# Performance work log

Hardware: AMD Instinct MI355X
Metric: run time of the kernel (lower is better)

Reference implementation:

```python
import jax, jax.numpy as jnp
import numpy as np

NUM_EXPERTS = 8
HIDDEN = 2048
EXPERT_DIM = 2048  # intermediate_size per shard (tp_size=1)
TOTAL_TOKENS = 32768  # divisible by NUM_EXPERTS


def setup_inputs() -> dict:
    key = jax.random.key(0)
    k1, k2, k3 = jax.random.split(key, 3)
    hidden_states = jax.random.normal(k1, (TOTAL_TOKENS, HIDDEN), dtype=jnp.float32)
    # (E, H, 2*D): gate and up projections concatenated on last dim
    gate_up_proj = jax.random.normal(k2, (NUM_EXPERTS, HIDDEN, 2 * EXPERT_DIM), dtype=jnp.float32) * 0.02
    # (E, D, H)
    down_proj = jax.random.normal(k3, (NUM_EXPERTS, EXPERT_DIM, HIDDEN), dtype=jnp.float32) * 0.02
    return {"hidden_states": hidden_states, "gate_up_proj": gate_up_proj, "down_proj": down_proj}


def reference(hidden_states, gate_up_proj, down_proj):
    E, H = gate_up_proj.shape[0], gate_up_proj.shape[1]
    # tokens are pre-sorted per expert: (E, T, H)
    x = hidden_states.reshape(E, -1, H)
    # grouped GEMM: (E,T,H) @ (E,H,2D) -> (E,T,2D)
    gate_up = jnp.einsum('eth,ehd->etd', x, gate_up_proj)
    gate, up = jnp.split(gate_up, 2, axis=-1)
    # SwiGLU epilogue then down projection: (E,T,D) @ (E,D,H) -> (E,T,H)
    act = up * jax.nn.silu(gate)
    out = jnp.einsum('etd,edh->eth', act, down_proj)
    # tp_size=1 -> all_reduce is identity
    return out.reshape(-1, H)
```

## Files before the change

kernel.cpp:

```cpp
#include <hip/hip_runtime.h>


#define E_EXPERTS 8
#define TPE 4096
#define KD 2048

typedef __bf16 bf16_t;
typedef __bf16 bf16x4 __attribute__((ext_vector_type(4)));
typedef __bf16 bf16x8 __attribute__((ext_vector_type(8)));
typedef float f32x4 __attribute__((ext_vector_type(4)));

#define GLOAD16(src, dst)                                               \
  __builtin_amdgcn_global_load_lds(                                     \
      (const __attribute__((address_space(1))) void*)(src),             \
      (__attribute__((address_space(3))) void*)(dst), 16, 0, 0)

__device__ inline void transpose64(const float* __restrict__ Wp,
                                   bf16_t* __restrict__ Tp, int N, int K,
                                   int n0, int k0, float (*tile)[65]) {
  const int rr = threadIdx.x >> 4;
  const int cc = (threadIdx.x & 15) * 4;
#pragma unroll
  for (int p = 0; p < 4; ++p) {
    const int k = rr + p * 16;
    float4 v = *(const float4*)(Wp + (size_t)(k0 + k) * N + n0 + cc);
    tile[k][cc + 0] = v.x;
    tile[k][cc + 1] = v.y;
    tile[k][cc + 2] = v.z;
    tile[k][cc + 3] = v.w;
  }
  __syncthreads();
#pragma unroll
  for (int p = 0; p < 4; ++p) {
    const int n = rr + p * 16;
    bf16x4 o;
#pragma unroll
    for (int q = 0; q < 4; ++q) o[q] = (bf16_t)tile[cc + q][n];
    *(bf16x4*)(Tp + (size_t)(n0 + n) * K + k0 + cc) = o;
  }
}

__global__ __launch_bounds__(256) void prep_kernel(
    const float* __restrict__ hs, bf16_t* __restrict__ xb,
    const float* __restrict__ w1, bf16_t* __restrict__ w1t,
    const float* __restrict__ w2, bf16_t* __restrict__ w2t) {
  __shared__ float tile[64][65];
  const int b = blockIdx.x;
  if (b < 16384) {
    const int nx = b & 63, ky = (b >> 6) & 31, e = b >> 11;
    transpose64(w1 + (size_t)e * KD * 4096, w1t + (size_t)e * 4096 * KD, 4096,
                KD, nx * 64, ky * 64, tile);
  } else if (b < 24576) {
    const int j = b - 16384;
    const int nx = j & 31, ky = (j >> 5) & 31, e = j >> 10;
    transpose64(w2 + (size_t)e * KD * KD, w2t + (size_t)e * KD * KD, KD, KD,
                nx * 64, ky * 64, tile);
  } else {
    const long n4 = (long)E_EXPERTS * TPE * KD / 4;
    long i = (long)(b - 24576) * blockDim.x + threadIdx.x;
    const long stride = 2048L * 256;
    const float4* in4 = (const float4*)hs;
    bf16x4* out4 = (bf16x4*)xb;
    for (; i < n4; i += stride) {
      float4 v = in4[i];
      bf16x4 o = {(bf16_t)v.x, (bf16_t)v.y, (bf16_t)v.z, (bf16_t)v.w};
      out4[i] = o;
    }
  }
}

template <bool FUSED, int NTN>
__global__ __launch_bounds__(512, 4) void moe_gemm_tlp_kernel(
    const bf16_t* __restrict__ A, const bf16_t* __restrict__ Bm,
    void* __restrict__ Cout) {
  constexpr int NT = KD / 32;

  __shared__ alignas(16) bf16_t As[3][64][64];
  __shared__ alignas(16) bf16_t Bs[3][128][64];

  const int NWG = gridDim.x;
  int wg = blockIdx.x;
  wg = (wg & 7) * (NWG >> 3) + (wg >> 3);
  const int e = wg / (32 * NTN);
  const int rem = wg % (32 * NTN);
  const int mt = rem / NTN, ntile = rem % NTN;
  const int t0 = mt * 128, n0 = ntile * 256;

  const int tid = threadIdx.x;
  const int wid = tid >> 6, lane = tid & 63;
  const int wr = wid >> 2, wc = wid & 3;

  const bf16_t* Ae = A + (size_t)e * TPE * KD + (size_t)t0 * KD;
  const bf16_t* Be = Bm + (size_t)e * (size_t)(FUSED ? 4096 : 2048) * KD;

  const int sp = lane >> 3;
  const int lc = lane & 7;

  const int pAr = wid * 8 + sp;
  const int cAr = lc ^ (pAr & 7);
  const bf16_t* aSrc = Ae + (size_t)(pAr + 64 * (cAr >> 2)) * KD + (cAr & 3) * 8;

  const bf16_t* bSrc[2];
#pragma unroll
  for (int i = 0; i < 2; ++i) {
    const int p = wid * 16 + i * 8 + sp;
    const int c = lc ^ (p & 7);
    const int R = n0 + p + 128 * (c >> 2);
    int srow;
    if constexpr (FUSED)
      srow = ((R >> 5) << 4) + (R & 15) + ((R >> 4) & 1) * 2048;
    else
      srow = R;
    bSrc[i] = Be + (size_t)srow * KD + (c & 3) * 8;
  }

  auto stageA = [&](int kt, int slot) {
    const int k0 = (kt & (NT - 1)) * 32;
    GLOAD16(aSrc + k0, &As[slot][wid * 8][0]);
  };
  auto stageB = [&](int kt, int slot) {
    const int k0 = (kt & (NT - 1)) * 32;
#pragma unroll
    for (int i = 0; i < 2; ++i)
      GLOAD16(bSrc[i] + k0, &Bs[slot][wid * 16 + i * 8][0]);
  };

  const int la = lane & 15, kg4 = lane >> 4;

  const bf16_t* pA[4];
#pragma unroll
  for (int m = 0; m < 4; ++m) {
    const int r = wr * 64 + m * 16 + la;
    const int p = r & 63, h = r >> 6;
    const int c = (h * 4 + kg4) ^ (p & 7);
    pA[m] = &As[0][p][c * 8];
  }
  const bf16_t* pB[4];
#pragma unroll
  for (int q = 0; q < 2; ++q)
#pragma unroll
    for (int jf = 0; jf < 2; ++jf) {
      const int R = wc * 64 + q * 32 + jf * 16 + la;
      const int p = R & 127, h = R >> 7;
      const int c = (h * 4 + kg4) ^ (p & 7);
      pB[q * 2 + jf] = &Bs[0][p][c * 8];
    }

  f32x4 acc[4][4] = {};
  bf16x8 am[4];
  bf16x8 bn[2];

#define W0 asm volatile("s_waitcnt lgkmcnt(0)" ::: "memory")
#define VMC3 asm volatile("s_waitcnt vmcnt(3)" ::: "memory")
#define BAR __builtin_amdgcn_s_barrier()
#define SCHED0 __builtin_amdgcn_sched_barrier(0)
#define PRIO1 __builtin_amdgcn_s_setprio(1)
#define PRIO0 __builtin_amdgcn_s_setprio(0)

#define TILE(t, S, S2)                                                       \
  do {                                                                       \
    am[0] = *(const bf16x8*)(pA[0] + (S) * 4096);                            \
    am[1] = *(const bf16x8*)(pA[1] + (S) * 4096);                            \
    am[2] = *(const bf16x8*)(pA[2] + (S) * 4096);                            \
    am[3] = *(const bf16x8*)(pA[3] + (S) * 4096);                            \
    bn[0] = *(const bf16x8*)(pB[0] + (S) * 8192);                            \
    bn[1] = *(const bf16x8*)(pB[1] + (S) * 8192);                            \
    stageA((t) + 2, S2);                                                     \
    stageB((t) + 2, S2);                                                     \
    W0; SCHED0;                                                              \
    PRIO1;                                                                   \
    _Pragma("unroll") for (int m = 0; m < 4; ++m) {                          \
      acc[m][0] = __builtin_amdgcn_mfma_f32_16x16x32_bf16(am[m], bn[0],      \
                                                          acc[m][0], 0, 0, 0); \
      acc[m][1] = __builtin_amdgcn_mfma_f32_16x16x32_bf16(am[m], bn[1],      \
                                                          acc[m][1], 0, 0, 0); \
    }                                                                        \
    PRIO0;                                                                   \
    bn[0] = *(const bf16x8*)(pB[2] + (S) * 8192);                            \
    bn[1] = *(const bf16x8*)(pB[3] + (S) * 8192);                            \
    W0; SCHED0;                                                              \
    PRIO1;                                                                   \
    _Pragma("unroll") for (int m = 0; m < 4; ++m) {                          \
      acc[m][2] = __builtin_amdgcn_mfma_f32_16x16x32_bf16(am[m], bn[0],      \
                                                          acc[m][2], 0, 0, 0); \
      acc[m][3] = __builtin_amdgcn_mfma_f32_16x16x32_bf16(am[m], bn[1],      \
                                                          acc[m][3], 0, 0, 0); \
    }                                                                        \
    PRIO0;                                                                   \
    VMC3;                                                                    \
    BAR; SCHED0;                                                             \
  } while (0)

  stageA(0, 0); stageB(0, 0);
  stageA(1, 1); stageB(1, 1);
  VMC3;
  BAR; SCHED0;

  int t = 0;
  for (; t < NT - 3; t += 3) {
    TILE(t, 0, 2);
    TILE(t + 1, 1, 0);
    TILE(t + 2, 2, 1);
  }
  TILE(t, 0, 2);

  const int rbase = t0 + wr * 64;
  if constexpr (FUSED) {
    bf16_t* Cp = (bf16_t*)Cout + (size_t)e * TPE * KD;
    const int jb = (n0 >> 1) + 32 * wc;
#pragma unroll
    for (int m = 0; m < 4; ++m)
#pragma unroll
      for (int q = 0; q < 2; ++q)
#pragma unroll
        for (int r = 0; r < 4; ++r) {
          const int row = rbase + m * 16 + kg4 * 4 + r;
          const int col = jb + q * 16 + la;
          const float g = acc[m][2 * q][r], u = acc[m][2 * q + 1][r];
          const float sg = 1.0f / (1.0f + __expf(-g));
          Cp[(size_t)row * KD + col] = (bf16_t)(u * g * sg);
        }
  } else {
    float* Cp = (float*)Cout + (size_t)e * TPE * KD;
#pragma unroll
    for (int m = 0; m < 4; ++m)
#pragma unroll
      for (int n = 0; n < 4; ++n)
#pragma unroll
        for (int r = 0; r < 4; ++r) {
          const int row = rbase + m * 16 + kg4 * 4 + r;
          const int col = n0 + wc * 64 + n * 16 + la;
          Cp[(size_t)row * KD + col] = acc[m][n][r];
        }
  }
#undef W0
#undef VMC3
#undef BAR
#undef SCHED0
#undef PRIO1
#undef PRIO0
#undef TILE
}

extern "C" void kernel_launch(void* const* d_in, const int* in_sizes, int n_in,
                              void* d_out, int out_size, void* d_ws,
                              size_t ws_size, hipStream_t stream) {
  const float* hs = (const float*)d_in[0];
  const float* w1 = (const float*)d_in[1];
  const float* w2 = (const float*)d_in[2];

  char* ws = (char*)d_ws;
  bf16_t* xb = (bf16_t*)(ws);
  bf16_t* w1t = (bf16_t*)(ws + (size_t)134217728);
  bf16_t* w2t = (bf16_t*)(ws + (size_t)268435456);
  bf16_t* act = (bf16_t*)(ws + (size_t)335544320);

  prep_kernel<<<26624, 256, 0, stream>>>(hs, xb, w1, w1t, w2, w2t);
  moe_gemm_tlp_kernel<true, 16><<<4096, 512, 0, stream>>>(xb, w1t, (void*)act);
  moe_gemm_tlp_kernel<false, 8><<<2048, 512, 0, stream>>>(act, w2t, d_out);
}
```

Before: 1.083 ms.

## Shrink GEMM tile to 128x128 with double-buffered LDS and higher occupancy

Reduces the per-workgroup output tile from 128x256 to 128x128 and switches from a triple-buffered to a double-buffered LDS pipeline with an extra barrier before staging. Launch bounds rise to 6 workgroups per CU and the grids double. The aim is more concurrent workgroups to hide latency. In exchange, each tile does less arithmetic per byte loaded, so global/LDS traffic per FLOP roughly rises, and the added barrier per k-step may cost throughput.

```diff
diff --git a/kernel.cpp b/kernel.cpp
--- a/kernel.cpp
+++ b/kernel.cpp
@@ -70,13 +70,13 @@
 }
 
 template <bool FUSED, int NTN>
-__global__ __launch_bounds__(512, 4) void moe_gemm_tlp_kernel(
+__global__ __launch_bounds__(512, 6) void moe_gemm128_kernel(
     const bf16_t* __restrict__ A, const bf16_t* __restrict__ Bm,
     void* __restrict__ Cout) {
   constexpr int NT = KD / 32;
 
-  __shared__ alignas(16) bf16_t As[3][64][64];
-  __shared__ alignas(16) bf16_t Bs[3][128][64];
+  __shared__ alignas(16) bf16_t As[2][64][64];
+  __shared__ alignas(16) bf16_t Bs[2][64][64];
 
   const int NWG = gridDim.x;
   int wg = blockIdx.x;
@@ -84,7 +84,7 @@
   const int e = wg / (32 * NTN);
   const int rem = wg % (32 * NTN);
   const int mt = rem / NTN, ntile = rem % NTN;
-  const int t0 = mt * 128, n0 = ntile * 256;
+  const int t0 = mt * 128, n0 = ntile * 128;
 
   const int tid = threadIdx.x;
   const int wid = tid >> 6, lane = tid & 63;
@@ -96,33 +96,25 @@
   const int sp = lane >> 3;
   const int lc = lane & 7;
 
-  const int pAr = wid * 8 + sp;
-  const int cAr = lc ^ (pAr & 7);
-  const bf16_t* aSrc = Ae + (size_t)(pAr + 64 * (cAr >> 2)) * KD + (cAr & 3) * 8;
-
-  const bf16_t* bSrc[2];
-#pragma unroll
-  for (int i = 0; i < 2; ++i) {
-    const int p = wid * 16 + i * 8 + sp;
-    const int c = lc ^ (p & 7);
-    const int R = n0 + p + 128 * (c >> 2);
+  const int pS = wid * 8 + sp;
+  const int cS = lc ^ (pS & 7);
+  const bf16_t* aSrc =
+      Ae + (size_t)(pS + 64 * (cS >> 2)) * KD + (cS & 3) * 8;
+  const bf16_t* bSrc;
+  {
+    const int R = n0 + pS + 64 * (cS >> 2);
     int srow;
     if constexpr (FUSED)
       srow = ((R >> 5) << 4) + (R & 15) + ((R >> 4) & 1) * 2048;
     else
       srow = R;
-    bSrc[i] = Be + (size_t)srow * KD + (c & 3) * 8;
-  }
-
-  auto stageA = [&](int kt, int slot) {
+    bSrc = Be + (size_t)srow * KD + (cS & 3) * 8;
+  }
+
+  auto stage = [&](int kt, int slot) {
     const int k0 = (kt & (NT - 1)) * 32;
     GLOAD16(aSrc + k0, &As[slot][wid * 8][0]);
-  };
-  auto stageB = [&](int kt, int slot) {
-    const int k0 = (kt & (NT - 1)) * 32;
-#pragma unroll
-    for (int i = 0; i < 2; ++i)
-      GLOAD16(bSrc[i] + k0, &Bs[slot][wid * 16 + i * 8][0]);
+    GLOAD16(bSrc + k0, &Bs[slot][wid * 8][0]);
   };
 
   const int la = lane & 15, kg4 = lane >> 4;
@@ -135,39 +127,37 @@
     const int c = (h * 4 + kg4) ^ (p & 7);
     pA[m] = &As[0][p][c * 8];
   }
-  const bf16_t* pB[4];
-#pragma unroll
-  for (int q = 0; q < 2; ++q)
-#pragma unroll
-    for (int jf = 0; jf < 2; ++jf) {
-      const int R = wc * 64 + q * 32 + jf * 16 + la;
-      const int p = R & 127, h = R >> 7;
-      const int c = (h * 4 + kg4) ^ (p & 7);
-      pB[q * 2 + jf] = &Bs[0][p][c * 8];
-    }
-
-  f32x4 acc[4][4] = {};
+  const bf16_t* pB[2];
+#pragma unroll
+  for (int nf = 0; nf < 2; ++nf) {
+    const int R = wc * 32 + nf * 16 + la;
+    const int p = R & 63, h = R >> 6;
+    const int c = (h * 4 + kg4) ^ (p & 7);
+    pB[nf] = &Bs[0][p][c * 8];
+  }
+
+  f32x4 acc[4][2] = {};
   bf16x8 am[4];
   bf16x8 bn[2];
 
 #define W0 asm volatile("s_waitcnt lgkmcnt(0)" ::: "memory")
-#define VMC3 asm volatile("s_waitcnt vmcnt(3)" ::: "memory")
+#define VMC2 asm volatile("s_waitcnt vmcnt(2)" ::: "memory")
 #define BAR __builtin_amdgcn_s_barrier()
 #define SCHED0 __builtin_amdgcn_sched_barrier(0)
 #define PRIO1 __builtin_amdgcn_s_setprio(1)
 #define PRIO0 __builtin_amdgcn_s_setprio(0)
 
-#define TILE(t, S, S2)                                                       \
+#define TILE(t, S)                                                           \
   do {                                                                       \
     am[0] = *(const bf16x8*)(pA[0] + (S) * 4096);                            \
     am[1] = *(const bf16x8*)(pA[1] + (S) * 4096);                            \
     am[2] = *(const bf16x8*)(pA[2] + (S) * 4096);                            \
     am[3] = *(const bf16x8*)(pA[3] + (S) * 4096);                            \
-    bn[0] = *(const bf16x8*)(pB[0] + (S) * 8192);                            \
-    bn[1] = *(const bf16x8*)(pB[1] + (S) * 8192);                            \
-    stageA((t) + 2, S2);                                                     \
-    stageB((t) + 2, S2);                                                     \
+    bn[0] = *(const bf16x8*)(pB[0] + (S) * 4096);                            \
+    bn[1] = *(const bf16x8*)(pB[1] + (S) * 4096);                            \
     W0; SCHED0;                                                              \
+    BAR;                                                                     \
+    stage((t) + 2, S);                                                       \
     PRIO1;                                                                   \
     _Pragma("unroll") for (int m = 0; m < 4; ++m) {                          \
       acc[m][0] = __builtin_amdgcn_mfma_f32_16x16x32_bf16(am[m], bn[0],      \
@@ -176,65 +166,49 @@
                                                           acc[m][1], 0, 0, 0); \
     }                                                                        \
     PRIO0;                                                                   \
-    bn[0] = *(const bf16x8*)(pB[2] + (S) * 8192);                            \
-    bn[1] = *(const bf16x8*)(pB[3] + (S) * 8192);                            \
-    W0; SCHED0;                                                              \
-    PRIO1;                                                                   \
-    _Pragma("unroll") for (int m = 0; m < 4; ++m) {                          \
-      acc[m][2] = __builtin_amdgcn_mfma_f32_16x16x32_bf16(am[m], bn[0],      \
-                                                          acc[m][2], 0, 0, 0); \
-      acc[m][3] = __builtin_amdgcn_mfma_f32_16x16x32_bf16(am[m], bn[1],      \
-                                                          acc[m][3], 0, 0, 0); \
-    }                                                                        \
-    PRIO0;                                                                   \
-    VMC3;                                                                    \
+    VMC2;                                                                    \
     BAR; SCHED0;                                                             \
   } while (0)
 
-  stageA(0, 0); stageB(0, 0);
-  stageA(1, 1); stageB(1, 1);
-  VMC3;
+  stage(0, 0);
+  stage(1, 1);
+  VMC2;
   BAR; SCHED0;
 
-  int t = 0;
-  for (; t < NT - 3; t += 3) {
-    TILE(t, 0, 2);
-    TILE(t + 1, 1, 0);
-    TILE(t + 2, 2, 1);
-  }
-  TILE(t, 0, 2);
+#pragma unroll 1
+  for (int t = 0; t < NT; t += 2) {
+    TILE(t, 0);
+    TILE(t + 1, 1);
+  }
 
   const int rbase = t0 + wr * 64;
   if constexpr (FUSED) {
     bf16_t* Cp = (bf16_t*)Cout + (size_t)e * TPE * KD;
-    const int jb = (n0 >> 1) + 32 * wc;
+    const int jb = ((n0 + wc * 32) >> 1) + la;
 #pragma unroll
     for (int m = 0; m < 4; ++m)
 #pragma unroll
-      for (int q = 0; q < 2; ++q)
+      for (int r = 0; r < 4; ++r) {
+        const int row = rbase + m * 16 + kg4 * 4 + r;
+        const float g = acc[m][0][r], u = acc[m][1][r];
+        const float sg = 1.0f / (1.0f + __expf(-g));
+        Cp[(size_t)row * KD + jb] = (bf16_t)(u * g * sg);
+      }
+  } else {
+    float* Cp = (float*)Cout + (size_t)e * TPE * KD;
+#pragma unroll
+    for (int m = 0; m < 4; ++m)
+#pragma unroll
+      for (int nf = 0; nf < 2; ++nf)
 #pragma unroll
         for (int r = 0; r < 4; ++r) {
           const int row = rbase + m * 16 + kg4 * 4 + r;
-          const int col = jb + q * 16 + la;
-          const float g = acc[m][2 * q][r], u = acc[m][2 * q + 1][r];
-          const float sg = 1.0f / (1.0f + __expf(-g));
-          Cp[(size_t)row * KD + col] = (bf16_t)(u * g * sg);
+          const int col = n0 + wc * 32 + nf * 16 + la;
+          Cp[(size_t)row * KD + col] = acc[m][nf][r];
         }
-  } else {
-    float* Cp = (float*)Cout + (size_t)e * TPE * KD;
-#pragma unroll
-    for (int m = 0; m < 4; ++m)
-#pragma unroll
-      for (int n = 0; n < 4; ++n)
-#pragma unroll
-        for (int r = 0; r < 4; ++r) {
-          const int row = rbase + m * 16 + kg4 * 4 + r;
-          const int col = n0 + wc * 64 + n * 16 + la;
-          Cp[(size_t)row * KD + col] = acc[m][n][r];
-        }
   }
 #undef W0
-#undef VMC3
+#undef VMC2
 #undef BAR
 #undef SCHED0
 #undef PRIO1
@@ -256,6 +230,6 @@
   bf16_t* act = (bf16_t*)(ws + (size_t)335544320);
 
   prep_kernel<<<26624, 256, 0, stream>>>(hs, xb, w1, w1t, w2, w2t);
-  moe_gemm_tlp_kernel<true, 16><<<4096, 512, 0, stream>>>(xb, w1t, (void*)act);
-  moe_gemm_tlp_kernel<false, 8><<<2048, 512, 0, stream>>>(act, w2t, d_out);
-}
+  moe_gemm128_kernel<true, 32><<<8192, 512, 0, stream>>>(xb, w1t, (void*)act);
+  moe_gemm128_kernel<false, 16><<<4096, 512, 0, stream>>>(act, w2t, d_out);
+}
```

After: 1.203 ms. 1.11x slower.

## Switch grouped GEMM inner loop to 32x32x16 bf16 MFMA tiles

Applied to the files above, without the earlier changes.

Replaces the 16x16x32 MFMA micro-tiles with 32x32x16 MFMA instructions, so each wave holds four 16-wide accumulators instead of sixteen 4-wide ones. The fused gate/up row interleave goes from 16-row to 32-row groups to match the new output fragment layout. LDS fragment loads are issued all at once with a partial lgkmcnt wait to overlap the second k-half. The goal is fewer LDS reads and MFMA issues per FLOP, with higher per-instruction latency and a different register and epilogue store pattern as the trade-off.

```diff
diff --git a/kernel.cpp b/kernel.cpp
--- a/kernel.cpp
+++ b/kernel.cpp
@@ -8,7 +8,7 @@
 typedef __bf16 bf16_t;
 typedef __bf16 bf16x4 __attribute__((ext_vector_type(4)));
 typedef __bf16 bf16x8 __attribute__((ext_vector_type(8)));
-typedef float f32x4 __attribute__((ext_vector_type(4)));
+typedef float f32x16 __attribute__((ext_vector_type(16)));
 
 #define GLOAD16(src, dst)                                               \
   __builtin_amdgcn_global_load_lds(                                     \
@@ -108,7 +108,7 @@
     const int R = n0 + p + 128 * (c >> 2);
     int srow;
     if constexpr (FUSED)
-      srow = ((R >> 5) << 4) + (R & 15) + ((R >> 4) & 1) * 2048;
+      srow = ((R >> 6) << 5) + (R & 31) + ((R >> 5) & 1) * 2048;
     else
       srow = R;
     bSrc[i] = Be + (size_t)srow * KD + (c & 3) * 8;
@@ -125,67 +125,69 @@
       GLOAD16(bSrc[i] + k0, &Bs[slot][wid * 16 + i * 8][0]);
   };
 
-  const int la = lane & 15, kg4 = lane >> 4;
-
-  const bf16_t* pA[4];
-#pragma unroll
-  for (int m = 0; m < 4; ++m) {
-    const int r = wr * 64 + m * 16 + la;
-    const int p = r & 63, h = r >> 6;
-    const int c = (h * 4 + kg4) ^ (p & 7);
-    pA[m] = &As[0][p][c * 8];
-  }
-  const bf16_t* pB[4];
-#pragma unroll
-  for (int q = 0; q < 2; ++q)
-#pragma unroll
-    for (int jf = 0; jf < 2; ++jf) {
-      const int R = wc * 64 + q * 32 + jf * 16 + la;
+  const int l31 = lane & 31, hk = lane >> 5;
+
+  const bf16_t* pA[2][2];
+#pragma unroll
+  for (int mf = 0; mf < 2; ++mf)
+#pragma unroll
+    for (int s = 0; s < 2; ++s) {
+      const int r = wr * 64 + mf * 32 + l31;
+      const int p = r & 63, h = r >> 6;
+      const int c = (h * 4 + 2 * s + hk) ^ (p & 7);
+      pA[mf][s] = &As[0][p][c * 8];
+    }
+  const bf16_t* pB[2][2];
+#pragma unroll
+  for (int nf = 0; nf < 2; ++nf)
+#pragma unroll
+    for (int s = 0; s < 2; ++s) {
+      const int R = wc * 64 + nf * 32 + l31;
       const int p = R & 127, h = R >> 7;
-      const int c = (h * 4 + kg4) ^ (p & 7);
-      pB[q * 2 + jf] = &Bs[0][p][c * 8];
+      const int c = (h * 4 + 2 * s + hk) ^ (p & 7);
+      pB[nf][s] = &Bs[0][p][c * 8];
     }
 
-  f32x4 acc[4][4] = {};
-  bf16x8 am[4];
-  bf16x8 bn[2];
-
+  f32x16 acc00 = {}, acc01 = {}, acc10 = {}, acc11 = {};
+  bf16x8 a0, a1, b0, b1;
+  bf16x8 a0n, a1n, b0n, b1n;
+
+#define W4 asm volatile("s_waitcnt lgkmcnt(4)" ::: "memory")
 #define W0 asm volatile("s_waitcnt lgkmcnt(0)" ::: "memory")
 #define VMC3 asm volatile("s_waitcnt vmcnt(3)" ::: "memory")
 #define BAR __builtin_amdgcn_s_barrier()
 #define SCHED0 __builtin_amdgcn_sched_barrier(0)
 #define PRIO1 __builtin_amdgcn_s_setprio(1)
 #define PRIO0 __builtin_amdgcn_s_setprio(0)
+#define MFMA32(ACC, AV, BV)                                                \
+  ACC = __builtin_amdgcn_mfma_f32_32x32x16_bf16(AV, BV, ACC, 0, 0, 0)
 
 #define TILE(t, S, S2)                                                       \
   do {                                                                       \
-    am[0] = *(const bf16x8*)(pA[0] + (S) * 4096);                            \
-    am[1] = *(const bf16x8*)(pA[1] + (S) * 4096);                            \
-    am[2] = *(const bf16x8*)(pA[2] + (S) * 4096);                            \
-    am[3] = *(const bf16x8*)(pA[3] + (S) * 4096);                            \
-    bn[0] = *(const bf16x8*)(pB[0] + (S) * 8192);                            \
-    bn[1] = *(const bf16x8*)(pB[1] + (S) * 8192);                            \
+                          \
+    a0 = *(const bf16x8*)(pA[0][0] + (S) * 4096);                            \
+    a1 = *(const bf16x8*)(pA[1][0] + (S) * 4096);                            \
+    b0 = *(const bf16x8*)(pB[0][0] + (S) * 8192);                            \
+    b1 = *(const bf16x8*)(pB[1][0] + (S) * 8192);                            \
+    a0n = *(const bf16x8*)(pA[0][1] + (S) * 4096);                           \
+    a1n = *(const bf16x8*)(pA[1][1] + (S) * 4096);                           \
+    b0n = *(const bf16x8*)(pB[0][1] + (S) * 8192);                           \
+    b1n = *(const bf16x8*)(pB[1][1] + (S) * 8192);                           \
     stageA((t) + 2, S2);                                                     \
     stageB((t) + 2, S2);                                                     \
+    W4; SCHED0;                                                              \
+    PRIO1;                                                                   \
+    MFMA32(acc00, a0, b0);                                                   \
+    MFMA32(acc01, a0, b1);                                                   \
+    MFMA32(acc10, a1, b0);                                                   \
+    MFMA32(acc11, a1, b1);                                                   \
+    PRIO0;                                                                   \
     W0; SCHED0;                                                              \
     PRIO1;                                                                   \
-    _Pragma("unroll") for (int m = 0; m < 4; ++m) {                          \
-      acc[m][0] = __builtin_amdgcn_mfma_f32_16x16x32_bf16(am[m], bn[0],      \
-                                                          acc[m][0], 0, 0, 0); \
-      acc[m][1] = __builtin_amdgcn_mfma_f32_16x16x32_bf16(am[m], bn[1],      \
-                                                          acc[m][1], 0, 0, 0); \
-    }                                                                        \
-    PRIO0;                                                                   \
-    bn[0] = *(const bf16x8*)(pB[2] + (S) * 8192);                            \
-    bn[1] = *(const bf16x8*)(pB[3] + (S) * 8192);                            \
-    W0; SCHED0;                                                              \
-    PRIO1;                                                                   \
-    _Pragma("unroll") for (int m = 0; m < 4; ++m) {                          \
-      acc[m][2] = __builtin_amdgcn_mfma_f32_16x16x32_bf16(am[m], bn[0],      \
-                                                          acc[m][2], 0, 0, 0); \
-      acc[m][3] = __builtin_amdgcn_mfma_f32_16x16x32_bf16(am[m], bn[1],      \
-                                                          acc[m][3], 0, 0, 0); \
-    }                                                                        \
+    MFMA32(acc00, a0n, b0n);                                                 \
+    MFMA32(acc01, a0n, b1n);                                                 \
+    MFMA32(acc10, a1n, b0n);                                                 \
+    MFMA32(acc11, a1n, b1n);                                                 \
     PRIO0;                                                                   \
     VMC3;                                                                    \
     BAR; SCHED0;                                                             \
@@ -207,38 +209,41 @@
   const int rbase = t0 + wr * 64;
   if constexpr (FUSED) {
     bf16_t* Cp = (bf16_t*)Cout + (size_t)e * TPE * KD;
-    const int jb = (n0 >> 1) + 32 * wc;
-#pragma unroll
-    for (int m = 0; m < 4; ++m)
-#pragma unroll
-      for (int q = 0; q < 2; ++q)
-#pragma unroll
-        for (int r = 0; r < 4; ++r) {
-          const int row = rbase + m * 16 + kg4 * 4 + r;
-          const int col = jb + q * 16 + la;
-          const float g = acc[m][2 * q][r], u = acc[m][2 * q + 1][r];
-          const float sg = 1.0f / (1.0f + __expf(-g));
-          Cp[(size_t)row * KD + col] = (bf16_t)(u * g * sg);
-        }
+    const int jb = (n0 >> 1) + wc * 32 + l31;
+    const f32x16* ag[2] = {&acc00, &acc10};
+    const f32x16* au[2] = {&acc01, &acc11};
+#pragma unroll
+    for (int mf = 0; mf < 2; ++mf)
+#pragma unroll
+      for (int reg = 0; reg < 16; ++reg) {
+        const int row = rbase + mf * 32 + (reg & 3) + 8 * (reg >> 2) + 4 * hk;
+        const float g = (*ag[mf])[reg], u = (*au[mf])[reg];
+        const float sg = 1.0f / (1.0f + __expf(-g));
+        Cp[(size_t)row * KD + jb] = (bf16_t)(u * g * sg);
+      }
   } else {
     float* Cp = (float*)Cout + (size_t)e * TPE * KD;
-#pragma unroll
-    for (int m = 0; m < 4; ++m)
-#pragma unroll
-      for (int n = 0; n < 4; ++n)
-#pragma unroll
-        for (int r = 0; r < 4; ++r) {
-          const int row = rbase + m * 16 + kg4 * 4 + r;
-          const int col = n0 + wc * 64 + n * 16 + la;
-          Cp[(size_t)row * KD + col] = acc[m][n][r];
+    const f32x16* am_[2][2] = {{&acc00, &acc01}, {&acc10, &acc11}};
+#pragma unroll
+    for (int mf = 0; mf < 2; ++mf)
+#pragma unroll
+      for (int nf = 0; nf < 2; ++nf)
+#pragma unroll
+        for (int reg = 0; reg < 16; ++reg) {
+          const int row =
+              rbase + mf * 32 + (reg & 3) + 8 * (reg >> 2) + 4 * hk;
+          const int col = n0 + wc * 64 + nf * 32 + l31;
+          Cp[(size_t)row * KD + col] = (*am_[mf][nf])[reg];
         }
   }
+#undef W4
 #undef W0
 #undef VMC3
 #undef BAR
 #undef SCHED0
 #undef PRIO1
 #undef PRIO0
+#undef MFMA32
 #undef TILE
 }
 
```

Result: slower. 1.173 ms (+8.3%).
